# Performance work log

Measured on AMD Instinct MI355X. Metric: run time of the kernel, lower is better.

Reference implementation:

```python
import jax, jax.numpy as jnp
import numpy as np

T_STEPS = 64   # number of actions (T-1 in the torch code)
BATCH = 512
STATE = 256
ACTION = 64
BELIEF = 1024
HIDDEN = 1024
EMB = 1024
MIN_STD = 0.1


def setup_inputs() -> dict:
    key = jax.random.key(0)
    ks = jax.random.split(key, 16)
    def w(k, shape):
        return jax.random.normal(k, shape, jnp.float32) * 0.02
    return {
        "s_0": jax.random.normal(ks[0], (BATCH, STATE), jnp.float32),
        "A": jax.random.normal(ks[1], (T_STEPS, BATCH, ACTION), jnp.float32),
        "b_0": jax.random.normal(ks[2], (BATCH, BELIEF), jnp.float32),
        "O": jax.random.normal(ks[3], (T_STEPS, BATCH, EMB), jnp.float32),
        "M": jnp.ones((T_STEPS, BATCH, 1), jnp.float32),
        "noise_pri": jax.random.normal(ks[4], (T_STEPS, BATCH, STATE), jnp.float32),
        "noise_pos": jax.random.normal(ks[5], (T_STEPS, BATCH, STATE), jnp.float32),
        # learned parameters (torch nn.Linear convention: y = x @ W.T + b)
        "W_sa": w(ks[6], (BELIEF, STATE + ACTION)), "b_sa": jnp.zeros((BELIEF,), jnp.float32),
        "W_ih": w(ks[7], (3 * BELIEF, BELIEF)), "b_ih": jnp.zeros((3 * BELIEF,), jnp.float32),
        "W_hh": w(ks[8], (3 * BELIEF, BELIEF)), "b_hh": jnp.zeros((3 * BELIEF,), jnp.float32),
        "W_bpri": w(ks[9], (HIDDEN, BELIEF)), "b_bpri": jnp.zeros((HIDDEN,), jnp.float32),
        "W_spri": w(ks[10], (2 * STATE, HIDDEN)), "b_spri": jnp.zeros((2 * STATE,), jnp.float32),
        "W_bpos": w(ks[11], (HIDDEN, BELIEF + EMB)), "b_bpos": jnp.zeros((HIDDEN,), jnp.float32),
        "W_spos": w(ks[12], (2 * STATE, HIDDEN)), "b_spos": jnp.zeros((2 * STATE,), jnp.float32),
    }


def reference(s_0, A, b_0, O, M, noise_pri, noise_pos,
              W_sa, b_sa, W_ih, b_ih, W_hh, b_hh,
              W_bpri, b_bpri, W_spri, b_spri,
              W_bpos, b_bpos, W_spos, b_spos):
    act = jax.nn.relu  # cfg.activation_function = 'relu'

    def gru_cell(x, h):
        # torch GRUCell gate order: r, z, n
        gi = x @ W_ih.T + b_ih      # [B, 3*BELIEF]
        gh = h @ W_hh.T + b_hh
        i_r, i_z, i_n = jnp.split(gi, 3, axis=1)
        h_r, h_z, h_n = jnp.split(gh, 3, axis=1)
        r = jax.nn.sigmoid(i_r + h_r)
        z = jax.nn.sigmoid(i_z + h_z)
        n = jnp.tanh(i_n + r * h_n)
        return (1.0 - z) * n + z * h

    def step(carry, xs):
        b, s = carry  # belief [B,BELIEF], posterior state [B,STATE]
        a_t, o_t, m_t, eps_p, eps_q = xs
        s_in = s * m_t  # non-terminal mask
        x = act(jnp.concatenate([s_in, a_t], axis=1) @ W_sa.T + b_sa)
        b_new = gru_cell(x, b)
        # prior
        pri = act(b_new @ W_bpri.T + b_bpri) @ W_spri.T + b_spri
        mu_p, hp = jnp.split(pri, 2, axis=1)
        std_p = jax.nn.softplus(hp) + MIN_STD
        s_p = mu_p + std_p * eps_p
        # posterior (uses current observation embedding)
        pos = act(jnp.concatenate([b_new, o_t], axis=1) @ W_bpos.T + b_bpos) @ W_spos.T + b_spos
        mu_q, hq = jnp.split(pos, 2, axis=1)
        std_q = jax.nn.softplus(hq) + MIN_STD
        s_q = mu_q + std_q * eps_q
        return (b_new, s_q), (b_new, s_p, mu_p, std_p, s_q, mu_q, std_q)

    (_, _), ys = jax.lax.scan(step, (b_0, s_0), (A, O, M, noise_pri, noise_pos))
    B_out, S_pri, MU_pri, STD_pri, S_pos, MU_pos, STD_pos = ys
    return B_out, S_pri, MU_pri, STD_pri, S_pos, MU_pos, STD_pos
```

## Files before the change

kernel.cpp:

```cpp
#include <hip/hip_runtime.h>
#include <hip/hip_bf16.h>
#include <math.h>

typedef short bf16x8 __attribute__((ext_vector_type(8)));
typedef float f32x4 __attribute__((ext_vector_type(4)));
typedef unsigned short u16;

#define NT 64
#define NB 512
#define NS 256
#define NA 64
#define NBEL 1024

#define OUT_B      0
#define OUT_SPRI   33554432
#define OUT_MUPRI  41943040
#define OUT_STDPRI 50331648
#define OUT_SPOS   58720256
#define OUT_MUPOS  67108864
#define OUT_STDPOS 75497472

__device__ __forceinline__ f32x4 mfma16(bf16x8 a, bf16x8 b, f32x4 c) {
  return __builtin_amdgcn_mfma_f32_16x16x32_bf16(a, b, c, 0, 0, 0);
}

__device__ __forceinline__ u16 f2bf(float f) {
  union { float f; unsigned u; } v; v.f = f;
  return (u16)((v.u + 0x7FFFu + ((v.u >> 16) & 1u)) >> 16);
}

__device__ __forceinline__ bf16x8 ld8bf(const u16* p) { return *(const bf16x8*)p; }

__device__ __forceinline__ bf16x8 cvt8(const float* p) {
  const float4 lo = *(const float4*)p;
  const float4 hi = *(const float4*)(p + 4);
  bf16x8 v;
  v[0] = (short)f2bf(lo.x); v[1] = (short)f2bf(lo.y);
  v[2] = (short)f2bf(lo.z); v[3] = (short)f2bf(lo.w);
  v[4] = (short)f2bf(hi.x); v[5] = (short)f2bf(hi.y);
  v[6] = (short)f2bf(hi.z); v[7] = (short)f2bf(hi.w);
  return v;
}

__device__ __forceinline__ float sigm(float x) { return 1.f / (1.f + __expf(-x)); }
__device__ __forceinline__ float softplus_(float x) {
  if (x > 20.f) return x;
  return log1pf(__expf(x));
}

#define ZACC(acc) { acc[0][0] = (f32x4){0.f,0.f,0.f,0.f}; acc[0][1] = (f32x4){0.f,0.f,0.f,0.f}; \
                    acc[1][0] = (f32x4){0.f,0.f,0.f,0.f}; acc[1][1] = (f32x4){0.f,0.f,0.f,0.f}; }

#define Q4(acc, a0v, a1v, b0v, b1v) \
  acc[0][0] = mfma16(a0v, b0v, acc[0][0]); \
  acc[0][1] = mfma16(a0v, b1v, acc[0][1]); \
  acc[1][0] = mfma16(a1v, b0v, acc[1][0]); \
  acc[1][1] = mfma16(a1v, b1v, acc[1][1]);

__device__ __forceinline__ void red_write(float* L, f32x4 (&acc)[2][2], int l) {
  const int base = l * 16;
#pragma unroll
  for (int i = 0; i < 2; ++i)
#pragma unroll
    for (int j = 0; j < 2; ++j)
#pragma unroll
      for (int q = 0; q < 4; ++q)
        L[base + (i * 2 + j) * 4 + q] = acc[i][j][q];
}
__device__ __forceinline__ void red_add(const float* L, f32x4 (&acc)[2][2], int l) {
  const int base = l * 16;
#pragma unroll
  for (int i = 0; i < 2; ++i)
#pragma unroll
    for (int j = 0; j < 2; ++j)
#pragma unroll
      for (int q = 0; q < 4; ++q)
        acc[i][j][q] += L[base + (i * 2 + j) * 4 + q];
}

__global__ __launch_bounds__(256) void cvt_weights_k(
    const float* __restrict__ wsa, const float* __restrict__ wih,
    const float* __restrict__ whh, const float* __restrict__ wbpri,
    const float* __restrict__ wspri, const float* __restrict__ wbpos,
    const float* __restrict__ wspos, u16* __restrict__ dst) {
  const int S0 = 327680;
  const int S1 = S0 + 3145728;
  const int S2 = S1 + 3145728;
  const int S3 = S2 + 1048576;
  const int S4 = S3 + 524288;
  const int S5 = S4 + 2097152;
  const int S6 = S5 + 524288;
  for (int i = blockIdx.x * blockDim.x + threadIdx.x; i < S6;
       i += gridDim.x * blockDim.x) {
    float v;
    if (i < S0) v = wsa[i];
    else if (i < S1) v = wih[i - S0];
    else if (i < S2) v = whh[i - S1];
    else if (i < S3) v = wbpri[i - S2];
    else if (i < S4) v = wspri[i - S3];
    else if (i < S5) v = wbpos[i - S4];
    else v = wspos[i - S5];
    dst[i] = f2bf(v);
  }
}

__global__ __launch_bounds__(256) void init_carry_k(
    const float* __restrict__ s0, const float* __restrict__ b0,
    const float* __restrict__ Mptr, u16* __restrict__ smask,
    u16* __restrict__ bbf0, float* __restrict__ hf) {
  for (int i = blockIdx.x * blockDim.x + threadIdx.x; i < NB * NBEL;
       i += gridDim.x * blockDim.x) {
    float b = b0[i];
    bbf0[i] = f2bf(b);
    hf[i] = b;
    if (i < NB * NS) {
      int row = i >> 8;
      smask[i] = f2bf(s0[i] * Mptr[row]);
    }
  }
}

__global__ __launch_bounds__(512, 2) void kA(
    const u16* __restrict__ smask, const float* __restrict__ Af,
    const u16* __restrict__ wsa, const float* __restrict__ bsa,
    u16* __restrict__ xbf, const float* __restrict__ Of,
    const u16* __restrict__ wbpos, float* __restrict__ hbO, int t) {
  __shared__ float lred[4][1024];
  const int l = threadIdx.x & 63, r16 = l & 15, kq = l >> 4;
  const int wid8 = threadIdx.x >> 6;
  const int wid = wid8 & 3, kh = wid8 >> 2;
  if (blockIdx.x < 128) {
    const int g = blockIdx.x, bm = g >> 4, bn = g & 15;
    const int row0 = bm * 64 + (wid >> 1) * 32;
    const int col0 = bn * 64 + (wid & 1) * 32;
    f32x4 acc[2][2]; ZACC(acc);
    const u16* A0 = smask + (row0 + r16) * NS + kq * 8;
    const u16* A1 = A0 + 16 * NS;
    const u16* B0 = wsa + (size_t)(col0 + r16) * 320 + kq * 8;
    const u16* B1 = B0 + 16 * 320;
    if (kh == 0) {
#pragma unroll
      for (int k = 0; k < 160; k += 32) {
        bf16x8 a0 = ld8bf(A0 + k), a1 = ld8bf(A1 + k);
        bf16x8 b0 = ld8bf(B0 + k), b1 = ld8bf(B1 + k);
        Q4(acc, a0, a1, b0, b1);
      }
    } else {
#pragma unroll
      for (int k = 160; k < 256; k += 32) {
        bf16x8 a0 = ld8bf(A0 + k), a1 = ld8bf(A1 + k);
        bf16x8 b0 = ld8bf(B0 + k), b1 = ld8bf(B1 + k);
        Q4(acc, a0, a1, b0, b1);
      }
      const float* F0 = Af + (size_t)t * (NB * NA) + (row0 + r16) * NA + kq * 8;
      const float* F1 = F0 + 16 * NA;
      const u16* C0 = wsa + (size_t)(col0 + r16) * 320 + 256 + kq * 8;
      const u16* C1 = C0 + 16 * 320;
#pragma unroll
      for (int k = 0; k < 64; k += 32) {
        bf16x8 a0 = cvt8(F0 + k), a1 = cvt8(F1 + k);
        bf16x8 b0 = ld8bf(C0 + k), b1 = ld8bf(C1 + k);
        Q4(acc, a0, a1, b0, b1);
      }
      red_write(lred[wid], acc, l);
    }
    __syncthreads();
    if (kh == 0) {
      red_add(lred[wid], acc, l);
#pragma unroll
      for (int i = 0; i < 2; ++i)
#pragma unroll
        for (int j = 0; j < 2; ++j)
#pragma unroll
          for (int q = 0; q < 4; ++q) {
            const int row = row0 + i * 16 + kq * 4 + q;
            const int col = col0 + j * 16 + r16;
            xbf[row * NBEL + col] = f2bf(fmaxf(acc[i][j][q] + bsa[col], 0.f));
          }
    }
  } else {
    const int g = blockIdx.x - 128, bm = g >> 4, bn = g & 15;
    const int row0 = bm * 64 + (wid >> 1) * 32;
    const int col0 = bn * 64 + (wid & 1) * 32;
    f32x4 acc[2][2]; ZACC(acc);
    const float* F0 = Of + (size_t)t * (NB * NBEL) + (row0 + r16) * NBEL + kh * 512 + kq * 8;
    const float* F1 = F0 + 16 * NBEL;
    const u16* B0 = wbpos + (size_t)(col0 + r16) * 2048 + 1024 + kh * 512 + kq * 8;
    const u16* B1 = B0 + 16 * 2048;
#pragma unroll 4
    for (int k = 0; k < 512; k += 32) {
      bf16x8 a0 = cvt8(F0 + k), a1 = cvt8(F1 + k);
      bf16x8 b0 = ld8bf(B0 + k), b1 = ld8bf(B1 + k);
      Q4(acc, a0, a1, b0, b1);
    }
    if (kh == 1) red_write(lred[wid], acc, l);
    __syncthreads();
    if (kh == 0) {
      red_add(lred[wid], acc, l);
#pragma unroll
      for (int i = 0; i < 2; ++i)
#pragma unroll
        for (int j = 0; j < 2; ++j)
#pragma unroll
          for (int q = 0; q < 4; ++q) {
            const int row = row0 + i * 16 + kq * 4 + q;
            const int col = col0 + j * 16 + r16;
            hbO[row * NBEL + col] = acc[i][j][q];
          }
    }
  }
}

__global__ __launch_bounds__(512, 2) void kB(
    const u16* __restrict__ xbf, const u16* __restrict__ bprev,
    const u16* __restrict__ wih, const u16* __restrict__ whh,
    const float* __restrict__ bih, const float* __restrict__ bhh,
    float* __restrict__ hf, u16* __restrict__ bcur, float* __restrict__ out,
    const u16* __restrict__ wbpri, const float* __restrict__ bbpri,
    u16* __restrict__ hpri, int t) {
  __shared__ float lred[4][3][1024];
  const int l = threadIdx.x & 63, r16 = l & 15, kq = l >> 4;
  const int wid8 = threadIdx.x >> 6;
  const int wid = wid8 & 3, kh = wid8 >> 2;
  if (blockIdx.x < 128) {
    if (t >= NT) return;
    const int g = blockIdx.x, bm = g >> 4, bn = g & 15;
    const int row0 = bm * 64 + (wid >> 1) * 32;
    const int col0 = bn * 64 + (wid & 1) * 32;
    f32x4 ar[2][2], az[2][2], an[2][2];
    ZACC(ar); ZACC(az); ZACC(an);
    const u16* Asrc = (kh == 0) ? xbf : bprev;
    const u16* W = (kh == 0) ? wih : whh;
    const u16* A0 = Asrc + (row0 + r16) * NBEL + kq * 8;
    const u16* A1 = A0 + 16 * NBEL;
    const u16* Br0 = W + (size_t)(col0 + r16) * NBEL + kq * 8;
    const u16* Br1 = Br0 + 16 * NBEL;
    const u16* Bz0 = W + (size_t)(col0 + 1024 + r16) * NBEL + kq * 8;
    const u16* Bz1 = Bz0 + 16 * NBEL;
    const u16* Bn0 = W + (size_t)(col0 + 2048 + r16) * NBEL + kq * 8;
    const u16* Bn1 = Bn0 + 16 * NBEL;
#pragma unroll 4
    for (int k = 0; k < NBEL; k += 32) {
      bf16x8 a0 = ld8bf(A0 + k), a1 = ld8bf(A1 + k);
      bf16x8 b0 = ld8bf(Br0 + k), b1 = ld8bf(Br1 + k);
      Q4(ar, a0, a1, b0, b1);
      bf16x8 c0 = ld8bf(Bz0 + k), c1 = ld8bf(Bz1 + k);
      Q4(az, a0, a1, c0, c1);
      bf16x8 d0 = ld8bf(Bn0 + k), d1 = ld8bf(Bn1 + k);
      Q4(an, a0, a1, d0, d1);
    }
    if (kh == 1) {
      red_write(lred[wid][0], ar, l);
      red_write(lred[wid][1], az, l);
      red_write(lred[wid][2], an, l);
    }
    __syncthreads();
    if (kh == 0) {
      const int base = l * 16;
#pragma unroll
      for (int i = 0; i < 2; ++i)
#pragma unroll
        for (int j = 0; j < 2; ++j)
#pragma unroll
          for (int q = 0; q < 4; ++q) {
            const int row = row0 + i * 16 + kq * 4 + q;
            const int c = col0 + j * 16 + r16;
            const int li = base + (i * 2 + j) * 4 + q;
            const float r = sigm(ar[i][j][q] + bih[c] + lred[wid][0][li] + bhh[c]);
            const float z = sigm(az[i][j][q] + bih[c + 1024] + lred[wid][1][li] + bhh[c + 1024]);
            const float n = tanhf(an[i][j][q] + bih[c + 2048] +
                                  r * (lred[wid][2][li] + bhh[c + 2048]));
            const float h = hf[row * NBEL + c];
            const float bnew = (1.f - z) * n + z * h;
            hf[row * NBEL + c] = bnew;
            bcur[row * NBEL + c] = f2bf(bnew);
            out[OUT_B + (size_t)t * (NB * NBEL) + row * NBEL + c] = bnew;
          }
    }
  } else {
    if (t < 1) return;
    const int g = blockIdx.x - 128, bm = g >> 4, bn = g & 15;
    const int row0 = bm * 64 + (wid >> 1) * 32;
    const int col0 = bn * 64 + (wid & 1) * 32;
    f32x4 acc[2][2]; ZACC(acc);
    const u16* A0 = bprev + (row0 + r16) * NBEL + kh * 512 + kq * 8;
    const u16* A1 = A0 + 16 * NBEL;
    const u16* B0 = wbpri + (size_t)(col0 + r16) * NBEL + kh * 512 + kq * 8;
    const u16* B1 = B0 + 16 * NBEL;
#pragma unroll 4
    for (int k = 0; k < 512; k += 32) {
      bf16x8 a0 = ld8bf(A0 + k), a1 = ld8bf(A1 + k);
      bf16x8 b0 = ld8bf(B0 + k), b1 = ld8bf(B1 + k);
      Q4(acc, a0, a1, b0, b1);
    }
    if (kh == 1) red_write(lred[wid][0], acc, l);
    __syncthreads();
    if (kh == 0) {
      red_add(lred[wid][0], acc, l);
#pragma unroll
      for (int i = 0; i < 2; ++i)
#pragma unroll
        for (int j = 0; j < 2; ++j)
#pragma unroll
          for (int q = 0; q < 4; ++q) {
            const int row = row0 + i * 16 + kq * 4 + q;
            const int col = col0 + j * 16 + r16;
            hpri[row * NBEL + col] = f2bf(fmaxf(acc[i][j][q] + bbpri[col], 0.f));
          }
    }
  }
}

__global__ __launch_bounds__(512, 2) void kC(
    const u16* __restrict__ bcur, const u16* __restrict__ wbpos,
    const float* __restrict__ bbpos, const float* __restrict__ hbO,
    u16* __restrict__ hbbf,
    const u16* __restrict__ hpri, const u16* __restrict__ wspri,
    const float* __restrict__ bspri, const float* __restrict__ npri,
    float* __restrict__ out, int t) {
  __shared__ float lred[4][2][1024];
  const int l = threadIdx.x & 63, r16 = l & 15, kq = l >> 4;
  const int wid8 = threadIdx.x >> 6;
  const int wid = wid8 & 3, kh = wid8 >> 2;
  if (blockIdx.x < 128) {
    if (t >= NT) return;
    const int g = blockIdx.x, bm = g >> 4, bn = g & 15;
    const int row0 = bm * 64 + (wid >> 1) * 32;
    const int col0 = bn * 64 + (wid & 1) * 32;
    f32x4 acc[2][2]; ZACC(acc);
    const u16* A0 = bcur + (row0 + r16) * NBEL + kh * 512 + kq * 8;
    const u16* A1 = A0 + 16 * NBEL;
    const u16* B0 = wbpos + (size_t)(col0 + r16) * 2048 + kh * 512 + kq * 8;
    const u16* B1 = B0 + 16 * 2048;
#pragma unroll 4
    for (int k = 0; k < 512; k += 32) {
      bf16x8 a0 = ld8bf(A0 + k), a1 = ld8bf(A1 + k);
      bf16x8 b0 = ld8bf(B0 + k), b1 = ld8bf(B1 + k);
      Q4(acc, a0, a1, b0, b1);
    }
    if (kh == 1) red_write(lred[wid][0], acc, l);
    __syncthreads();
    if (kh == 0) {
      red_add(lred[wid][0], acc, l);
#pragma unroll
      for (int i = 0; i < 2; ++i)
#pragma unroll
        for (int j = 0; j < 2; ++j)
#pragma unroll
          for (int q = 0; q < 4; ++q) {
            const int row = row0 + i * 16 + kq * 4 + q;
            const int col = col0 + j * 16 + r16;
            const float v = acc[i][j][q] + hbO[row * NBEL + col] + bbpos[col];
            hbbf[row * NBEL + col] = f2bf(fmaxf(v, 0.f));
          }
    }
  } else {
    if (t < 1) return;
    const int g = blockIdx.x - 128, bm = g >> 2, bn = g & 3;
    const int row0 = bm * 64 + (wid >> 1) * 32;
    const int c0 = bn * 64 + (wid & 1) * 32;
    f32x4 am[2][2], ah[2][2];
    ZACC(am); ZACC(ah);
    const u16* A0 = hpri + (row0 + r16) * NBEL + kh * 512 + kq * 8;
    const u16* A1 = A0 + 16 * NBEL;
    const u16* Bm0 = wspri + (size_t)(c0 + r16) * NBEL + kh * 512 + kq * 8;
    const u16* Bm1 = Bm0 + 16 * NBEL;
    const u16* Bh0 = wspri + (size_t)(c0 + 256 + r16) * NBEL + kh * 512 + kq * 8;
    const u16* Bh1 = Bh0 + 16 * NBEL;
#pragma unroll 4
    for (int k = 0; k < 512; k += 32) {
      bf16x8 a0 = ld8bf(A0 + k), a1 = ld8bf(A1 + k);
      bf16x8 m0 = ld8bf(Bm0 + k), m1 = ld8bf(Bm1 + k);
      Q4(am, a0, a1, m0, m1);
      bf16x8 h0 = ld8bf(Bh0 + k), h1 = ld8bf(Bh1 + k);
      Q4(ah, a0, a1, h0, h1);
    }
    if (kh == 1) {
      red_write(lred[wid][0], am, l);
      red_write(lred[wid][1], ah, l);
    }
    __syncthreads();
    if (kh == 0) {
      red_add(lred[wid][0], am, l);
      red_add(lred[wid][1], ah, l);
      const int tt = t - 1;
#pragma unroll
      for (int i = 0; i < 2; ++i)
#pragma unroll
        for (int j = 0; j < 2; ++j)
#pragma unroll
          for (int q = 0; q < 4; ++q) {
            const int row = row0 + i * 16 + kq * 4 + q;
            const int c = c0 + j * 16 + r16;
            const size_t idx = (size_t)tt * (NB * NS) + row * NS + c;
            const float mu = am[i][j][q] + bspri[c];
            const float hp = ah[i][j][q] + bspri[c + 256];
            const float sd = softplus_(hp) + 0.1f;
            out[OUT_SPRI + idx] = mu + sd * npri[idx];
            out[OUT_MUPRI + idx] = mu;
            out[OUT_STDPRI + idx] = sd;
          }
    }
  }
}

__global__ __launch_bounds__(512, 2) void kD(
    const u16* __restrict__ hbbf, const u16* __restrict__ wspos,
    const float* __restrict__ bspos, const float* __restrict__ npos,
    const float* __restrict__ Mptr, float* __restrict__ out,
    u16* __restrict__ smask, int t) {
  __shared__ float lred[4][2][1024];
  const int l = threadIdx.x & 63, r16 = l & 15, kq = l >> 4;
  const int wid8 = threadIdx.x >> 6;
  const int wid = wid8 & 3, kh = wid8 >> 2;
  const int g = blockIdx.x, bm = g >> 2, bn = g & 3;
  const int row0 = bm * 64 + (wid >> 1) * 32;
  const int c0 = bn * 64 + (wid & 1) * 32;
  f32x4 am[2][2], ah[2][2];
  ZACC(am); ZACC(ah);
  const u16* A0 = hbbf + (row0 + r16) * NBEL + kh * 512 + kq * 8;
  const u16* A1 = A0 + 16 * NBEL;
  const u16* Bm0 = wspos + (size_t)(c0 + r16) * NBEL + kh * 512 + kq * 8;
  const u16* Bm1 = Bm0 + 16 * NBEL;
  const u16* Bh0 = wspos + (size_t)(c0 + 256 + r16) * NBEL + kh * 512 + kq * 8;
  const u16* Bh1 = Bh0 + 16 * NBEL;
#pragma unroll 4
  for (int k = 0; k < 512; k += 32) {
    bf16x8 a0 = ld8bf(A0 + k), a1 = ld8bf(A1 + k);
    bf16x8 m0 = ld8bf(Bm0 + k), m1 = ld8bf(Bm1 + k);
    Q4(am, a0, a1, m0, m1);
    bf16x8 h0 = ld8bf(Bh0 + k), h1 = ld8bf(Bh1 + k);
    Q4(ah, a0, a1, h0, h1);
  }
  if (kh == 1) {
    red_write(lred[wid][0], am, l);
    red_write(lred[wid][1], ah, l);
  }
  __syncthreads();
  if (kh == 0) {
    red_add(lred[wid][0], am, l);
    red_add(lred[wid][1], ah, l);
#pragma unroll
    for (int i = 0; i < 2; ++i)
#pragma unroll
      for (int j = 0; j < 2; ++j)
#pragma unroll
        for (int q = 0; q < 4; ++q) {
          const int row = row0 + i * 16 + kq * 4 + q;
          const int c = c0 + j * 16 + r16;
          const float mu = am[i][j][q] + bspos[c];
          const float hq = ah[i][j][q] + bspos[c + 256];
          const float sd = softplus_(hq) + 0.1f;
          const size_t idx = (size_t)t * (NB * NS) + row * NS + c;
          const float sq = mu + sd * npos[idx];
          out[OUT_SPOS + idx] = sq;
          out[OUT_MUPOS + idx] = mu;
          out[OUT_STDPOS + idx] = sd;
          const float mn = (t < NT - 1) ? Mptr[(t + 1) * NB + row] : 1.f;
          smask[row * NS + c] = f2bf(sq * mn);
        }
  }
}

extern "C" void kernel_launch(void* const* d_in, const int* in_sizes, int n_in,
                              void* d_out, int out_size, void* d_ws, size_t ws_size,
                              hipStream_t stream) {
  const float* s0 = (const float*)d_in[0];
  const float* Af = (const float*)d_in[1];
  const float* b0 = (const float*)d_in[2];
  const float* Of = (const float*)d_in[3];
  const float* Mp = (const float*)d_in[4];
  const float* npri = (const float*)d_in[5];
  const float* npos = (const float*)d_in[6];
  const float* Wsa = (const float*)d_in[7];
  const float* bsa = (const float*)d_in[8];
  const float* Wih = (const float*)d_in[9];
  const float* bih = (const float*)d_in[10];
  const float* Whh = (const float*)d_in[11];
  const float* bhh = (const float*)d_in[12];
  const float* Wbpri = (const float*)d_in[13];
  const float* bbpri = (const float*)d_in[14];
  const float* Wspri = (const float*)d_in[15];
  const float* bspri = (const float*)d_in[16];
  const float* Wbpos = (const float*)d_in[17];
  const float* bbpos = (const float*)d_in[18];
  const float* Wspos = (const float*)d_in[19];
  const float* bspos = (const float*)d_in[20];

  float* out = (float*)d_out;
  char* ws = (char*)d_ws;
  u16* wbase   = (u16*)ws;
  u16* wsa_b   = wbase;
  u16* wih_b   = wbase + 327680;
  u16* whh_b   = wbase + 3473408;
  u16* wbpri_b = wbase + 6619136;
  u16* wspri_b = wbase + 7667712;
  u16* wbpos_b = wbase + 8192000;
  u16* wspos_b = wbase + 10289152;
  u16*   smask = (u16*)  (ws + 21626880);
  u16*   bbf0  = (u16*)  (ws + 21889024);
  u16*   bbf1  = (u16*)  (ws + 22937600);
  float* hf    = (float*)(ws + 23986176);
  u16*   xbf   = (u16*)  (ws + 26083328);
  float* hbO   = (float*)(ws + 27131904);
  u16*   hbbf  = (u16*)  (ws + 29229056);
  u16*   hpri  = (u16*)  (ws + 30277632);

  cvt_weights_k<<<2048, 256, 0, stream>>>(Wsa, Wih, Whh, Wbpri, Wspri, Wbpos,
                                          Wspos, wbase);
  init_carry_k<<<2048, 256, 0, stream>>>(s0, b0, Mp, smask, bbf0, hf);

  for (int t = 0; t < NT; ++t) {
    const u16* bprev = (t & 1) ? bbf1 : bbf0;
    u16* bcur = (t & 1) ? bbf0 : bbf1;
    kA<<<256, 512, 0, stream>>>(smask, Af, wsa_b, bsa, xbf, Of, wbpos_b, hbO, t);
    kB<<<256, 512, 0, stream>>>(xbf, bprev, wih_b, whh_b, bih, bhh, hf, bcur,
                                out, wbpri_b, bbpri, hpri, t);
    kC<<<160, 512, 0, stream>>>(bcur, wbpos_b, bbpos, hbO, hbbf,
                                hpri, wspri_b, bspri, npri, out, t);
    kD<<<32, 512, 0, stream>>>(hbbf, wspos_b, bspos, npos, Mp, out, smask, t);
  }
  {
    const int t = NT;
    const u16* bprev = (t & 1) ? bbf1 : bbf0;
    u16* bcur = (t & 1) ? bbf0 : bbf1;
    kB<<<256, 512, 0, stream>>>(xbf, bprev, wih_b, whh_b, bih, bhh, hf, bcur,
                                out, wbpri_b, bbpri, hpri, t);
    kC<<<160, 512, 0, stream>>>(bcur, wbpos_b, bbpos, hbO, hbbf,
                                hpri, wspri_b, bspri, npri, out, t);
  }
}
```

Measured before the change: 10.06 ms.

## Replace per-step kernel launches with a persistent cooperative kernel using flag dataflow

Adds a single persistent cooperative kernel that runs the whole 64-step scan, with blocks assigned fixed roles per XCD and coordinated by atomic counters instead of the previous four launches per step. It also reorganises the pipeline: the observation half of the posterior GEMM is precomputed one step ahead, input and hidden GRU gate GEMMs are split across separate blocks, and prior heads are computed lagged to overlap with the next step. The intent is to remove launch overhead and global barriers, and to overlap independent GEMMs across the recurrence. It risks spin-wait deadlock or ordering bugs and relies on the cooperative launch succeeding, otherwise it falls back to the old path.

```diff
diff --git a/kernel.cpp b/kernel.cpp
--- a/kernel.cpp
+++ b/kernel.cpp
@@ -20,6 +20,7 @@
 #define OUT_MUPOS  67108864
 #define OUT_STDPOS 75497472
 
+
 __device__ __forceinline__ f32x4 mfma16(bf16x8 a, bf16x8 b, f32x4 c) {
   return __builtin_amdgcn_mfma_f32_16x16x32_bf16(a, b, c, 0, 0, 0);
 }
@@ -27,6 +28,9 @@
 __device__ __forceinline__ u16 f2bf(float f) {
   union { float f; unsigned u; } v; v.f = f;
   return (u16)((v.u + 0x7FFFu + ((v.u >> 16) & 1u)) >> 16);
+}
+__device__ __forceinline__ float bf2f(u16 h) {
+  union { unsigned u; float f; } v; v.u = ((unsigned)h) << 16; return v.f;
 }
 
 __device__ __forceinline__ bf16x8 ld8bf(const u16* p) { return *(const bf16x8*)p; }
@@ -57,25 +61,47 @@
   acc[1][0] = mfma16(a1v, b0v, acc[1][0]); \
   acc[1][1] = mfma16(a1v, b1v, acc[1][1]);
 
-__device__ __forceinline__ void red_write(float* L, f32x4 (&acc)[2][2], int l) {
-  const int base = l * 16;
-#pragma unroll
-  for (int i = 0; i < 2; ++i)
-#pragma unroll
-    for (int j = 0; j < 2; ++j)
-#pragma unroll
-      for (int q = 0; q < 4; ++q)
-        L[base + (i * 2 + j) * 4 + q] = acc[i][j][q];
-}
-__device__ __forceinline__ void red_add(const float* L, f32x4 (&acc)[2][2], int l) {
-  const int base = l * 16;
-#pragma unroll
-  for (int i = 0; i < 2; ++i)
-#pragma unroll
-    for (int j = 0; j < 2; ++j)
-#pragma unroll
-      for (int q = 0; q < 4; ++q)
-        acc[i][j][q] += L[base + (i * 2 + j) * 4 + q];
+__device__ __forceinline__ void gtile(f32x4 (&acc)[2][2],
+    const u16* __restrict__ A, int lda, const u16* __restrict__ B, int ldb,
+    int K, int r16, int kq) {
+  const u16* A0 = A + r16 * lda + kq * 8;
+  const u16* A1 = A0 + 16 * lda;
+  const u16* B0 = B + (size_t)r16 * ldb + kq * 8;
+  const u16* B1 = B0 + 16 * ldb;
+#pragma unroll 4
+  for (int k = 0; k < K; k += 32) {
+    bf16x8 a0 = ld8bf(A0 + k), a1 = ld8bf(A1 + k);
+    bf16x8 b0 = ld8bf(B0 + k), b1 = ld8bf(B1 + k);
+    Q4(acc, a0, a1, b0, b1);
+  }
+}
+__device__ __forceinline__ void gtileF(f32x4 (&acc)[2][2],
+    const float* __restrict__ A, int lda, const u16* __restrict__ B, int ldb,
+    int K, int r16, int kq) {
+  const float* A0 = A + r16 * lda + kq * 8;
+  const float* A1 = A0 + 16 * lda;
+  const u16* B0 = B + (size_t)r16 * ldb + kq * 8;
+  const u16* B1 = B0 + 16 * ldb;
+#pragma unroll 2
+  for (int k = 0; k < K; k += 32) {
+    bf16x8 a0 = cvt8(A0 + k), a1 = cvt8(A1 + k);
+    bf16x8 b0 = ld8bf(B0 + k), b1 = ld8bf(B1 + k);
+    Q4(acc, a0, a1, b0, b1);
+  }
+}
+
+__device__ __forceinline__ void setflag(unsigned* f) {
+  __syncthreads();
+  if (threadIdx.x == 0)
+    __hip_atomic_fetch_add(f, 1u, __ATOMIC_RELEASE, __HIP_MEMORY_SCOPE_AGENT);
+}
+__device__ __forceinline__ void waitflag(unsigned* f, unsigned target) {
+  if (threadIdx.x == 0) {
+    while (__hip_atomic_load(f, __ATOMIC_RELAXED, __HIP_MEMORY_SCOPE_AGENT) < target)
+      __builtin_amdgcn_s_sleep(2);
+    (void)__hip_atomic_load(f, __ATOMIC_ACQUIRE, __HIP_MEMORY_SCOPE_AGENT);
+  }
+  __syncthreads();
 }
 
 __global__ __launch_bounds__(256) void cvt_weights_k(
@@ -102,6 +128,367 @@
     else v = wspos[i - S5];
     dst[i] = f2bf(v);
   }
+}
+
+__global__ __launch_bounds__(256) void init2_k(
+    const float* __restrict__ s0, const float* __restrict__ b0,
+    const float* __restrict__ Mptr, u16* __restrict__ smaskg,
+    u16* __restrict__ bn1, float* __restrict__ hfX,
+    unsigned* __restrict__ flags) {
+  for (int i = blockIdx.x * blockDim.x + threadIdx.x; i < NB * NBEL;
+       i += gridDim.x * blockDim.x) {
+    const int row = i >> 10, c = i & 1023;
+    const float b = b0[i];
+    bn1[i] = f2bf(b);
+    hfX[(((size_t)(c >> 7)) * 512 + row) * 128 + (c & 127)] = b;
+    if (i < NB * NS) {
+      const int r2 = i >> 8;
+      smaskg[i] = f2bf(s0[i] * Mptr[r2]);
+    }
+    if (i < 2040) {
+      unsigned v = 0;
+      if (i < 408) {
+        const int kind = i / 68, tt = i % 68;
+        if (tt == 0 && kind == 1) v = 128;
+        else if (tt == 0 && (kind == 3 || kind == 5)) v = 64;
+      }
+      flags[i] = v;
+    }
+  }
+}
+
+struct SP2 {
+  const float *Af, *Of, *Mp, *npri, *npos;
+  const float *bsa, *bih, *bhh, *bbpri, *bspri, *bbpos, *bspos;
+  const u16 *wsa, *wih, *whh, *wbpri, *wspri, *wbpos, *wspos;
+  float *out;
+  u16 *smaskg, *xg, *bn0, *bn1, *hbg, *hprig, *hbo, *ghX;
+  float *giX, *hfX;
+  unsigned *flagsG, *flagsL;
+};
+
+__global__ void __launch_bounds__(256, 2) rssm_scan2(SP2 p) {
+  const int slot = blockIdx.x >> 3;
+  const int xcd  = blockIdx.x & 7;
+  const int l = threadIdx.x & 63, r16 = l & 15, kq = l >> 4;
+  const int wid = threadIdx.x >> 6;
+  const int qr = (wid >> 1) * 32, qc = (wid & 1) * 32;
+  __shared__ float sp_lds[2][64][32];
+
+#define FGp(k, tt) (p.flagsG + (k) * 68 + (tt))
+#define FLp(k, tt) (p.flagsL + (xcd * 3 + (k)) * 68 + (tt))
+
+  if (slot >= 16 && slot < 32) {
+    const int s = slot - 16;
+    const int row0 = (s >> 1) * 64 + qr;
+    const int cl0 = (s & 1) * 64 + qc;
+    const int colw = xcd * 128 + cl0;
+    f32x4 acc[2][2]; ZACC(acc);
+    gtileF(acc, p.Of + (size_t)row0 * NBEL, NBEL,
+           p.wbpos + (size_t)colw * 2048 + 1024, 2048, 1024, r16, kq);
+    u16* dst = p.hbo + ((size_t)xcd * 2 + 0) * 65536;
+#pragma unroll
+    for (int ii = 0; ii < 2; ++ii)
+#pragma unroll
+      for (int jj = 0; jj < 2; ++jj)
+#pragma unroll
+        for (int qq = 0; qq < 4; ++qq) {
+          const int row = row0 + ii * 16 + kq * 4 + qq;
+          dst[row * 128 + cl0 + jj * 16 + r16] = f2bf(acc[ii][jj][qq]);
+        }
+    setflag(FLp(0, 0));
+  }
+
+  for (int t = 0; t <= NT; ++t) {
+    u16* bcur = (t & 1) ? p.bn1 : p.bn0;
+    const u16* bprev = (t & 1) ? p.bn0 : p.bn1;
+
+    if (slot < 16) {
+      if (t < NT) {
+        waitflag(FGp(5, t), 64);
+        const int s = slot;
+        const int row0 = (s >> 1) * 64 + qr;
+        const int cl0 = (s & 1) * 64 + qc;
+        const int colw = xcd * 128 + cl0;
+        f32x4 acc[2][2]; ZACC(acc);
+        gtile(acc, p.smaskg + row0 * 256, 256,
+              p.wsa + (size_t)colw * 320, 320, 256, r16, kq);
+        gtileF(acc, p.Af + (size_t)t * (NB * NA) + (size_t)row0 * NA, NA,
+               p.wsa + (size_t)colw * 320 + 256, 320, 64, r16, kq);
+#pragma unroll
+        for (int ii = 0; ii < 2; ++ii)
+#pragma unroll
+          for (int jj = 0; jj < 2; ++jj)
+#pragma unroll
+            for (int qq = 0; qq < 4; ++qq) {
+              const int row = row0 + ii * 16 + kq * 4 + qq;
+              const int col = colw + jj * 16 + r16;
+              p.xg[row * 1024 + col] = f2bf(fmaxf(acc[ii][jj][qq] + p.bsa[col], 0.f));
+            }
+        setflag(FGp(0, t));
+      }
+    } else if (slot < 32) {
+      if (t + 1 < NT) {
+        if (t >= 1) waitflag(FGp(4, t - 1), 128);
+        const int s = slot - 16;
+        const int row0 = (s >> 1) * 64 + qr;
+        const int cl0 = (s & 1) * 64 + qc;
+        const int colw = xcd * 128 + cl0;
+        f32x4 acc[2][2]; ZACC(acc);
+        gtileF(acc, p.Of + (size_t)(t + 1) * (NB * NBEL) + (size_t)row0 * NBEL, NBEL,
+               p.wbpos + (size_t)colw * 2048 + 1024, 2048, 1024, r16, kq);
+        u16* dst = p.hbo + ((size_t)xcd * 2 + ((t + 1) & 1)) * 65536;
+#pragma unroll
+        for (int ii = 0; ii < 2; ++ii)
+#pragma unroll
+          for (int jj = 0; jj < 2; ++jj)
+#pragma unroll
+            for (int qq = 0; qq < 4; ++qq) {
+              const int row = row0 + ii * 16 + kq * 4 + qq;
+              dst[row * 128 + cl0 + jj * 16 + r16] = f2bf(acc[ii][jj][qq]);
+            }
+        setflag(FLp(0, t + 1));
+      }
+    }
+
+    if (t < NT) {
+      if (slot < 48) {
+        waitflag(FGp(1, t), 128);
+        const int G = slot >> 4, s = slot & 15;
+        const int row0 = (s >> 1) * 64 + qr;
+        const int cl0 = (s & 1) * 64 + qc;
+        const int colw = G * 1024 + xcd * 128 + cl0;
+        f32x4 acc[2][2]; ZACC(acc);
+        gtile(acc, bprev + row0 * 1024, 1024,
+              p.whh + (size_t)colw * 1024, 1024, 1024, r16, kq);
+#pragma unroll
+        for (int ii = 0; ii < 2; ++ii)
+#pragma unroll
+          for (int jj = 0; jj < 2; ++jj)
+#pragma unroll
+            for (int qq = 0; qq < 4; ++qq) {
+              const int row = row0 + ii * 16 + kq * 4 + qq;
+              const int jc = jj * 16 + r16;
+              p.ghX[((size_t)xcd * 512 + row) * 384 + G * 128 + cl0 + jc] =
+                  f2bf(acc[ii][jj][qq] + p.bhh[colw + jc]);
+            }
+        setflag(FLp(2, t));
+      } else {
+        waitflag(FGp(0, t), 128);
+        const int i0 = slot - 48;
+        const int G = i0 >> 4, s = i0 & 15;
+        const int row0 = (s >> 1) * 64 + qr;
+        const int cl0 = (s & 1) * 64 + qc;
+        const int colw = G * 1024 + xcd * 128 + cl0;
+        f32x4 acc[2][2]; ZACC(acc);
+        gtile(acc, p.xg + row0 * 1024, 1024,
+              p.wih + (size_t)colw * 1024, 1024, 1024, r16, kq);
+#pragma unroll
+        for (int ii = 0; ii < 2; ++ii)
+#pragma unroll
+          for (int jj = 0; jj < 2; ++jj)
+#pragma unroll
+            for (int qq = 0; qq < 4; ++qq) {
+              const int row = row0 + ii * 16 + kq * 4 + qq;
+              const int jc = jj * 16 + r16;
+              p.giX[((size_t)xcd * 512 + row) * 384 + G * 128 + cl0 + jc] =
+                  acc[ii][jj][qq] + p.bih[colw + jc];
+            }
+        setflag(FLp(1, t));
+      }
+      if (slot < 32) {
+        waitflag(FGp(0, t), 128);
+        const int i0 = 16 + slot;
+        const int G = i0 >> 4, s = i0 & 15;
+        const int row0 = (s >> 1) * 64 + qr;
+        const int cl0 = (s & 1) * 64 + qc;
+        const int colw = G * 1024 + xcd * 128 + cl0;
+        f32x4 acc[2][2]; ZACC(acc);
+        gtile(acc, p.xg + row0 * 1024, 1024,
+              p.wih + (size_t)colw * 1024, 1024, 1024, r16, kq);
+#pragma unroll
+        for (int ii = 0; ii < 2; ++ii)
+#pragma unroll
+          for (int jj = 0; jj < 2; ++jj)
+#pragma unroll
+            for (int qq = 0; qq < 4; ++qq) {
+              const int row = row0 + ii * 16 + kq * 4 + qq;
+              const int jc = jj * 16 + r16;
+              p.giX[((size_t)xcd * 512 + row) * 384 + G * 128 + cl0 + jc] =
+                  acc[ii][jj][qq] + p.bih[colw + jc];
+            }
+        setflag(FLp(1, t));
+      }
+    }
+
+    if (slot >= 32 && slot < 48 && t >= 1) {
+      waitflag(FGp(1, t), 128);
+      waitflag(FGp(3, t - 1), 64);
+      const int s = slot - 32;
+      const int row0 = (s >> 1) * 64 + qr;
+      const int cl0 = (s & 1) * 64 + qc;
+      const int colw = xcd * 128 + cl0;
+      f32x4 acc[2][2]; ZACC(acc);
+      gtile(acc, bprev + row0 * 1024, 1024,
+            p.wbpri + (size_t)colw * 1024, 1024, 1024, r16, kq);
+#pragma unroll
+      for (int ii = 0; ii < 2; ++ii)
+#pragma unroll
+        for (int jj = 0; jj < 2; ++jj)
+#pragma unroll
+          for (int qq = 0; qq < 4; ++qq) {
+            const int row = row0 + ii * 16 + kq * 4 + qq;
+            const int col = colw + jj * 16 + r16;
+            p.hprig[row * 1024 + col] = f2bf(fmaxf(acc[ii][jj][qq] + p.bbpri[col], 0.f));
+          }
+      setflag(FGp(2, t));
+    }
+
+    if (slot >= 48 && slot < 56 && t >= 1) {
+      waitflag(FGp(2, t), 128);
+      const int s = slot - 48;
+      const int gem = wid & 1, rh = wid >> 1;
+      f32x4 acc[2][2]; ZACC(acc);
+      gtile(acc, p.hprig + (size_t)(s * 64 + rh * 32) * 1024, 1024,
+            p.wspri + (size_t)((gem ? 256 : 0) + xcd * 32) * 1024, 1024, 1024, r16, kq);
+#pragma unroll
+      for (int ii = 0; ii < 2; ++ii)
+#pragma unroll
+        for (int jj = 0; jj < 2; ++jj)
+#pragma unroll
+          for (int qq = 0; qq < 4; ++qq)
+            sp_lds[gem][rh * 32 + ii * 16 + kq * 4 + qq][jj * 16 + r16] = acc[ii][jj][qq];
+      __syncthreads();
+      const int rr = threadIdx.x >> 2;
+      const int cb = (threadIdx.x & 3) * 8;
+      const int tt = t - 1;
+      const int row = s * 64 + rr;
+#pragma unroll
+      for (int e = 0; e < 8; ++e) {
+        const int cl = cb + e;
+        const int c = xcd * 32 + cl;
+        const float mu = sp_lds[0][rr][cl] + p.bspri[c];
+        const float hp = sp_lds[1][rr][cl] + p.bspri[256 + c];
+        const float sd = softplus_(hp) + 0.1f;
+        const size_t idx = (size_t)tt * (NB * NS) + (size_t)row * NS + c;
+        p.out[OUT_SPRI + idx] = mu + sd * p.npri[idx];
+        p.out[OUT_MUPRI + idx] = mu;
+        p.out[OUT_STDPRI + idx] = sd;
+      }
+      setflag(FGp(3, t));
+    }
+
+    if (slot < 16 && t < NT) {
+      waitflag(FLp(1, t), 48);
+      waitflag(FLp(2, t), 48);
+      if (t >= 2) waitflag(FGp(2, t - 1), 128);
+      const int rl = threadIdx.x >> 3;
+      const int row = slot * 32 + rl;
+      const int cl0 = (threadIdx.x & 7) * 16;
+      const float* gi = p.giX + ((size_t)xcd * 512 + row) * 384;
+      const u16* gh = p.ghX + ((size_t)xcd * 512 + row) * 384;
+      float* hr = p.hfX + ((size_t)xcd * 512 + row) * 128;
+      float* orow = p.out + OUT_B + (size_t)t * (NB * NBEL) + (size_t)row * NBEL;
+#pragma unroll 4
+      for (int e = 0; e < 16; ++e) {
+        const int cl = cl0 + e;
+        const int c = xcd * 128 + cl;
+        const float r = sigm(gi[cl] + bf2f(gh[cl]));
+        const float z = sigm(gi[128 + cl] + bf2f(gh[128 + cl]));
+        const float n = tanhf(gi[256 + cl] + r * bf2f(gh[256 + cl]));
+        const float h = hr[cl];
+        const float bnew = (1.f - z) * n + z * h;
+        hr[cl] = bnew;
+        bcur[row * 1024 + c] = f2bf(bnew);
+        orow[c] = bnew;
+      }
+      setflag(FGp(1, t + 1));
+    }
+
+    if (slot >= 16 && slot < 32 && t < NT) {
+      waitflag(FGp(1, t + 1), 128);
+      waitflag(FLp(0, t), 16);
+      const int s = slot - 16;
+      const int row0 = (s >> 1) * 64 + qr;
+      const int cl0 = (s & 1) * 64 + qc;
+      const int colw = xcd * 128 + cl0;
+      f32x4 acc[2][2]; ZACC(acc);
+      gtile(acc, bcur + row0 * 1024, 1024,
+            p.wbpos + (size_t)colw * 2048, 2048, 1024, r16, kq);
+      const u16* ho = p.hbo + ((size_t)xcd * 2 + (t & 1)) * 65536;
+#pragma unroll
+      for (int ii = 0; ii < 2; ++ii)
+#pragma unroll
+        for (int jj = 0; jj < 2; ++jj)
+#pragma unroll
+          for (int qq = 0; qq < 4; ++qq) {
+            const int row = row0 + ii * 16 + kq * 4 + qq;
+            const int cl = cl0 + jj * 16 + r16;
+            const float v = acc[ii][jj][qq] + bf2f(ho[row * 128 + cl]) + p.bbpos[xcd * 128 + cl];
+            p.hbg[row * 1024 + xcd * 128 + cl] = f2bf(fmaxf(v, 0.f));
+          }
+      setflag(FGp(4, t));
+    }
+
+    if (slot >= 56 && t < NT) {
+      waitflag(FGp(4, t), 128);
+      const int s = slot - 56;
+      const int gem = wid & 1, rh = wid >> 1;
+      f32x4 acc[2][2]; ZACC(acc);
+      gtile(acc, p.hbg + (size_t)(s * 64 + rh * 32) * 1024, 1024,
+            p.wspos + (size_t)((gem ? 256 : 0) + xcd * 32) * 1024, 1024, 1024, r16, kq);
+#pragma unroll
+      for (int ii = 0; ii < 2; ++ii)
+#pragma unroll
+        for (int jj = 0; jj < 2; ++jj)
+#pragma unroll
+          for (int qq = 0; qq < 4; ++qq)
+            sp_lds[gem][rh * 32 + ii * 16 + kq * 4 + qq][jj * 16 + r16] = acc[ii][jj][qq];
+      __syncthreads();
+      const int rr = threadIdx.x >> 2;
+      const int cb = (threadIdx.x & 3) * 8;
+      const int row = s * 64 + rr;
+#pragma unroll
+      for (int e = 0; e < 8; ++e) {
+        const int cl = cb + e;
+        const int c = xcd * 32 + cl;
+        const float mu = sp_lds[0][rr][cl] + p.bspos[c];
+        const float hq = sp_lds[1][rr][cl] + p.bspos[256 + c];
+        const float sd = softplus_(hq) + 0.1f;
+        const size_t idx = (size_t)t * (NB * NS) + (size_t)row * NS + c;
+        const float sq = mu + sd * p.npos[idx];
+        p.out[OUT_SPOS + idx] = sq;
+        p.out[OUT_MUPOS + idx] = mu;
+        p.out[OUT_STDPOS + idx] = sd;
+        const float mn = (t < NT - 1) ? p.Mp[(t + 1) * NB + row] : 1.f;
+        p.smaskg[row * 256 + c] = f2bf(sq * mn);
+      }
+      setflag(FGp(5, t + 1));
+    }
+  }
+#undef FGp
+#undef FLp
+}
+
+__device__ __forceinline__ void red_write(float* L, f32x4 (&acc)[2][2], int l) {
+  const int base = l * 16;
+#pragma unroll
+  for (int i = 0; i < 2; ++i)
+#pragma unroll
+    for (int j = 0; j < 2; ++j)
+#pragma unroll
+      for (int q = 0; q < 4; ++q)
+        L[base + (i * 2 + j) * 4 + q] = acc[i][j][q];
+}
+__device__ __forceinline__ void red_add(const float* L, f32x4 (&acc)[2][2], int l) {
+  const int base = l * 16;
+#pragma unroll
+  for (int i = 0; i < 2; ++i)
+#pragma unroll
+    for (int j = 0; j < 2; ++j)
+#pragma unroll
+      for (int q = 0; q < 4; ++q)
+        acc[i][j][q] += L[base + (i * 2 + j) * 4 + q];
 }
 
 __global__ __launch_bounds__(256) void init_carry_k(
@@ -250,9 +637,9 @@
       Q4(an, a0, a1, d0, d1);
     }
     if (kh == 1) {
-      red_write(lred[wid][0], ar, l);
-      red_write(lred[wid][1], az, l);
-      red_write(lred[wid][2], an, l);
+      red_write(&lred[wid][0][0], ar, l);
+      red_write(&lred[wid][1][0], az, l);
+      red_write(&lred[wid][2][0], an, l);
     }
     __syncthreads();
     if (kh == 0) {
@@ -293,10 +680,10 @@
       bf16x8 b0 = ld8bf(B0 + k), b1 = ld8bf(B1 + k);
       Q4(acc, a0, a1, b0, b1);
     }
-    if (kh == 1) red_write(lred[wid][0], acc, l);
+    if (kh == 1) red_write(&lred[wid][0][0], acc, l);
     __syncthreads();
     if (kh == 0) {
-      red_add(lred[wid][0], acc, l);
+      red_add(&lred[wid][0][0], acc, l);
 #pragma unroll
       for (int i = 0; i < 2; ++i)
 #pragma unroll
@@ -338,10 +725,10 @@
       bf16x8 b0 = ld8bf(B0 + k), b1 = ld8bf(B1 + k);
       Q4(acc, a0, a1, b0, b1);
     }
-    if (kh == 1) red_write(lred[wid][0], acc, l);
+    if (kh == 1) red_write(&lred[wid][0][0], acc, l);
     __syncthreads();
     if (kh == 0) {
-      red_add(lred[wid][0], acc, l);
+      red_add(&lred[wid][0][0], acc, l);
 #pragma unroll
       for (int i = 0; i < 2; ++i)
 #pragma unroll
@@ -376,13 +763,13 @@
       Q4(ah, a0, a1, h0, h1);
     }
     if (kh == 1) {
-      red_write(lred[wid][0], am, l);
-      red_write(lred[wid][1], ah, l);
+      red_write(&lred[wid][0][0], am, l);
+      red_write(&lred[wid][1][0], ah, l);
     }
     __syncthreads();
     if (kh == 0) {
-      red_add(lred[wid][0], am, l);
-      red_add(lred[wid][1], ah, l);
+      red_add(&lred[wid][0][0], am, l);
+      red_add(&lred[wid][1][0], ah, l);
       const int tt = t - 1;
 #pragma unroll
       for (int i = 0; i < 2; ++i)
@@ -433,13 +820,13 @@
     Q4(ah, a0, a1, h0, h1);
   }
   if (kh == 1) {
-    red_write(lred[wid][0], am, l);
-    red_write(lred[wid][1], ah, l);
+    red_write(&lred[wid][0][0], am, l);
+    red_write(&lred[wid][1][0], ah, l);
   }
   __syncthreads();
   if (kh == 0) {
-    red_add(lred[wid][0], am, l);
-    red_add(lred[wid][1], ah, l);
+    red_add(&lred[wid][0][0], am, l);
+    red_add(&lred[wid][1][0], ah, l);
 #pragma unroll
     for (int i = 0; i < 2; ++i)
 #pragma unroll
@@ -497,6 +884,42 @@
   u16* wspri_b = wbase + 7667712;
   u16* wbpos_b = wbase + 8192000;
   u16* wspos_b = wbase + 10289152;
+
+  unsigned* flagsG = (unsigned*)(ws + 21626880);
+  unsigned* flagsL = (unsigned*)(ws + 21626880 + 1632);
+  u16*   smaskg = (u16*)  (ws + 21643264);
+  u16*   xg     = (u16*)  (ws + 21905408);
+  u16*   bn0    = (u16*)  (ws + 22953984);
+  u16*   bn1    = (u16*)  (ws + 24002560);
+  u16*   hbg    = (u16*)  (ws + 25051136);
+  u16*   hprig  = (u16*)  (ws + 26099712);
+  u16*   hbo    = (u16*)  (ws + 27148288);
+  float* giX    = (float*)(ws + 29245440);
+  u16*   ghX    = (u16*)  (ws + 35536896);
+  float* hfX    = (float*)(ws + 38682624);
+
+  cvt_weights_k<<<2048, 256, 0, stream>>>(Wsa, Wih, Whh, Wbpri, Wspri, Wbpos,
+                                          Wspos, wbase);
+  init2_k<<<2048, 256, 0, stream>>>(s0, b0, Mp, smaskg, bn1, hfX, flagsG);
+
+  SP2 p;
+  p.Af = Af; p.Of = Of; p.Mp = Mp; p.npri = npri; p.npos = npos;
+  p.bsa = bsa; p.bih = bih; p.bhh = bhh; p.bbpri = bbpri; p.bspri = bspri;
+  p.bbpos = bbpos; p.bspos = bspos;
+  p.wsa = wsa_b; p.wih = wih_b; p.whh = whh_b; p.wbpri = wbpri_b;
+  p.wspri = wspri_b; p.wbpos = wbpos_b; p.wspos = wspos_b;
+  p.out = out;
+  p.smaskg = smaskg; p.xg = xg; p.bn0 = bn0; p.bn1 = bn1;
+  p.hbg = hbg; p.hprig = hprig; p.hbo = hbo; p.ghX = ghX;
+  p.giX = giX; p.hfX = hfX;
+  p.flagsG = flagsG; p.flagsL = flagsL;
+
+  void* args[] = {(void*)&p};
+  hipError_t err = hipLaunchCooperativeKernel(
+      reinterpret_cast<const void*>(&rssm_scan2), dim3(512), dim3(256),
+      args, 0, stream);
+  if (err == hipSuccess) return;
+
   u16*   smask = (u16*)  (ws + 21626880);
   u16*   bbf0  = (u16*)  (ws + 21889024);
   u16*   bbf1  = (u16*)  (ws + 22937600);
@@ -506,10 +929,7 @@
   u16*   hbbf  = (u16*)  (ws + 29229056);
   u16*   hpri  = (u16*)  (ws + 30277632);
 
-  cvt_weights_k<<<2048, 256, 0, stream>>>(Wsa, Wih, Whh, Wbpri, Wspri, Wbpos,
-                                          Wspos, wbase);
   init_carry_k<<<2048, 256, 0, stream>>>(s0, b0, Mp, smask, bbf0, hf);
-
   for (int t = 0; t < NT; ++t) {
     const u16* bprev = (t & 1) ? bbf1 : bbf0;
     u16* bcur = (t & 1) ? bbf0 : bbf1;
```

Result: slower. 14.46 ms (+43.8%).
